# Optimization experiments

Measured on AMD Instinct MI355X. Metric: run time of the kernel, lower is better.

The kernel has to match this reference:

```python
import jax, jax.numpy as jnp
import numpy as np

ALPHA = 0.1
EPS = 1e-10

def setup_inputs() -> dict:
    key = jax.random.key(0)
    k1, k2 = jax.random.split(key)
    x = jax.random.normal(k1, (64, 8192, 128), dtype=jnp.float32)   # [B, N, D]
    pv = jax.random.uniform(k2, (64, 128), dtype=jnp.float32)        # [M, D] prototypes (torch.rand init)
    return {"x": x, "pv": pv}

def _cdist(x, pv):
    # Euclidean pairwise distance via GEMM form: [B,N,D] x [M,D] -> [B,N,M]
    x2 = jnp.sum(x * x, axis=-1, keepdims=True)          # [B,N,1]
    p2 = jnp.sum(pv * pv, axis=-1)                        # [M]
    xp = jnp.einsum('bnd,md->bnm', x, pv)                 # [B,N,M]
    return jnp.sqrt(jnp.maximum(x2 + p2 - 2.0 * xp, 0.0))

def reference(x, pv):
    dist = _cdist(x, pv)                                  # [B,N,M]
    min_dist = jnp.min(dist, axis=1)                      # [B,M] closest patch per prototype
    min_pos = jnp.argmin(dist, axis=1)                    # [B,M]
    # pick, per batch, the patch position of the globally closest prototype (no-grad in original)
    idx = jnp.argmin(min_dist, axis=1)                    # [B]
    min_pos = min_pos[jnp.arange(min_pos.shape[0]), idx]  # [B]
    max_sim = jnp.exp(EPS - ALPHA * min_dist)             # [B,M]
    return (max_sim, min_pos)
```

## Files before the change

### kernel.cpp

```cpp
#include <hip/hip_runtime.h>
#include <cfloat>
#include <cmath>

#define B_ 64
#define N_ 8192
#define D_ 128
#define M_ 64
#define CROWS 64
#define NCHUNK 4
#define BROWS (CROWS*NCHUNK)
#define NBLK (N_/BROWS)
#define ALPHA_ 0.1f
#define EPS_ 1e-10f

typedef __attribute__((ext_vector_type(4))) float f32x4;
typedef __attribute__((ext_vector_type(8))) short bf16x8;
typedef __attribute__((ext_vector_type(4))) short s16x4;

static __device__ __forceinline__ short f2bf(float f) {
    unsigned u = __float_as_uint(f);
    u += 0x7fff + ((u >> 16) & 1);
    return (short)(u >> 16);
}
static __device__ __forceinline__ float bf2f(short s) {
    return __uint_as_float(((unsigned)(unsigned short)s) << 16);
}

__global__ __launch_bounds__(256, 2)
void protomin_mfma(const float* __restrict__ x, const float* __restrict__ pv,
                   float* __restrict__ wsv, int* __restrict__ wsa) {
    __shared__ short xhi[2][CROWS * D_];
    __shared__ short xlo[2][CROWS * D_];
    __shared__ float x2s[2][CROWS];
    __shared__ float redv[2][M_];
    __shared__ int   redp[2][M_];

    const int tid = threadIdx.x;
    const int w   = tid >> 6;
    const int l   = tid & 63;
    const int lm  = l & 15, lg = l >> 4;
    const int wr  = w & 1;
    const int wm  = w >> 1;
    const int bid = blockIdx.x;
    const int b   = bid >> 5;
    const int nbase = (bid & 31) * BROWS;

    const float* xblk = x + ((size_t)b * N_ + nbase) * D_;

    f32x4 nv[8];
    {
        const f32x4* src = (const f32x4*)xblk;
#pragma unroll
        for (int i = 0; i < 8; ++i) nv[i] = src[(w * 8 + i) * 64 + l];
    }

    bf16x8 Bh[2][4], Bl[2][4];
#pragma unroll
    for (int mti = 0; mti < 2; ++mti) {
#pragma unroll
        for (int kt = 0; kt < 4; ++kt) {
            const float* p = pv + (wm * 32 + mti * 16 + lm) * D_ + kt * 32 + lg * 8;
            f32x4 p0 = *(const f32x4*)p;
            f32x4 p1 = *(const f32x4*)(p + 4);
#pragma unroll
            for (int j = 0; j < 4; ++j) {
                short h = f2bf(p0[j]);
                Bh[mti][kt][j] = h;
                Bl[mti][kt][j] = f2bf(p0[j] - bf2f(h));
            }
#pragma unroll
            for (int j = 0; j < 4; ++j) {
                short h = f2bf(p1[j]);
                Bh[mti][kt][4 + j] = h;
                Bl[mti][kt][4 + j] = f2bf(p1[j] - bf2f(h));
            }
        }
    }

    auto stage = [&](int buf) {
#pragma unroll
        for (int i = 0; i < 8; ++i) {
            int seg = w * 8 + i;
            int row = seg * 2 + (l >> 5);
            int ks  = (l & 31) * 4;
            f32x4 v = nv[i];
            float s = v[0] * v[0];
            s = fmaf(v[1], v[1], s); s = fmaf(v[2], v[2], s); s = fmaf(v[3], v[3], s);
            s += __shfl_xor(s, 1);  s += __shfl_xor(s, 2);  s += __shfl_xor(s, 4);
            s += __shfl_xor(s, 8);  s += __shfl_xor(s, 16);
            if ((l & 31) == 0) x2s[buf][row] = s;
            s16x4 hv, lv;
#pragma unroll
            for (int j = 0; j < 4; ++j) {
                short h = f2bf(v[j]);
                hv[j] = h;
                lv[j] = f2bf(v[j] - bf2f(h));
            }
            int sidx = row * D_ + (ks ^ ((row & 7) << 3));
            *(s16x4*)&xhi[buf][sidx] = hv;
            *(s16x4*)&xlo[buf][sidx] = lv;
        }
    };

    float bv[2]; int bp[2];
#pragma unroll
    for (int mti = 0; mti < 2; ++mti) { bv[mti] = FLT_MAX; bp[mti] = 0; }

    stage(0);
    __syncthreads();

    for (int c = 0; c < NCHUNK; ++c) {
        const int cur = c & 1;
        if (c + 1 < NCHUNK) {
            const f32x4* src = (const f32x4*)(xblk + (size_t)(c + 1) * CROWS * D_);
#pragma unroll
            for (int i = 0; i < 8; ++i) nv[i] = src[(w * 8 + i) * 64 + l];
        }

        f32x4 acc[2][2] = {};
#pragma unroll
        for (int kt = 0; kt < 4; ++kt) {
            bf16x8 ah[2], al[2];
#pragma unroll
            for (int rt = 0; rt < 2; ++rt) {
                int arow = wr * 32 + rt * 16 + lm;
                int koff = (kt * 32 + lg * 8) ^ ((arow & 7) << 3);
                ah[rt] = *(const bf16x8*)&xhi[cur][arow * D_ + koff];
                al[rt] = *(const bf16x8*)&xlo[cur][arow * D_ + koff];
            }
#pragma unroll
            for (int rt = 0; rt < 2; ++rt) {
#pragma unroll
                for (int mti = 0; mti < 2; ++mti) {
                    acc[rt][mti] = __builtin_amdgcn_mfma_f32_16x16x32_bf16(ah[rt], Bh[mti][kt], acc[rt][mti], 0, 0, 0);
                    acc[rt][mti] = __builtin_amdgcn_mfma_f32_16x16x32_bf16(al[rt], Bh[mti][kt], acc[rt][mti], 0, 0, 0);
                    acc[rt][mti] = __builtin_amdgcn_mfma_f32_16x16x32_bf16(ah[rt], Bl[mti][kt], acc[rt][mti], 0, 0, 0);
                    acc[rt][mti] = __builtin_amdgcn_mfma_f32_16x16x32_bf16(al[rt], Bl[mti][kt], acc[rt][mti], 0, 0, 0);
                }
            }
        }

#pragma unroll
        for (int rt = 0; rt < 2; ++rt) {
            const int rbase = wr * 32 + rt * 16 + lg * 4;
            float x2v[4];
#pragma unroll
            for (int r = 0; r < 4; ++r) x2v[r] = x2s[cur][rbase + r];
            const int npos0 = nbase + c * CROWS + rbase;
#pragma unroll
            for (int mti = 0; mti < 2; ++mti) {
#pragma unroll
                for (int r = 0; r < 4; ++r) {
                    float cand = fmaf(-2.f, acc[rt][mti][r], x2v[r]);
                    if (cand < bv[mti]) { bv[mti] = cand; bp[mti] = npos0 + r; }
                }
            }
        }

        if (c + 1 < NCHUNK) stage(cur ^ 1);
        __syncthreads();
    }

#pragma unroll
    for (int mti = 0; mti < 2; ++mti) {
        float v = bv[mti]; int p = bp[mti];
#pragma unroll
        for (int off = 16; off <= 32; off <<= 1) {
            float ov = __shfl_xor(v, off);
            int   op = __shfl_xor(p, off);
            if (ov < v || (ov == v && op < p)) { v = ov; p = op; }
        }
        if (l < 16) { redv[wr][wm * 32 + mti * 16 + l] = v;
                      redp[wr][wm * 32 + mti * 16 + l] = p; }
    }
    __syncthreads();

    if (tid < M_) {
        float v = redv[0][tid]; int p = redp[0][tid];
        float ov = redv[1][tid]; int op = redp[1][tid];
        if (ov < v || (ov == v && op < p)) { v = ov; p = op; }
        wsv[(size_t)bid * M_ + tid] = v;
        wsa[(size_t)bid * M_ + tid] = p;
    }
}

__global__ void finalize_kernel(const float* __restrict__ wsv,
                                const int* __restrict__ wsa,
                                const float* __restrict__ pv,
                                float* __restrict__ out) {
    const int b = blockIdx.x;
    const int m = threadIdx.x;

    float p2 = 0.f;
    const f32x4* pp = (const f32x4*)(pv + m * D_);
#pragma unroll 8
    for (int j = 0; j < 32; ++j) {
        f32x4 v = pp[j];
        p2 = fmaf(v[0], v[0], p2); p2 = fmaf(v[1], v[1], p2);
        p2 = fmaf(v[2], v[2], p2); p2 = fmaf(v[3], v[3], p2);
    }

    float v = FLT_MAX; int p = 0;
    for (int bc = 0; bc < NBLK; ++bc) {
        size_t idx = ((size_t)(b * NBLK + bc)) * M_ + m;
        float nv2 = wsv[idx]; int np = wsa[idx];
        if (nv2 < v || (nv2 == v && np < p)) { v = nv2; p = np; }
    }
    float dist = sqrtf(fmaxf(v + p2, 0.f));
    out[b * M_ + m] = expf(EPS_ - ALPHA_ * dist);

    __shared__ float sv[M_];
    __shared__ int   sa[M_];
    sv[m] = dist; sa[m] = p;
    __syncthreads();
    if (m == 0) {
        float best = FLT_MAX; int bpos = 0;
        for (int k = 0; k < M_; ++k)
            if (sv[k] < best) { best = sv[k]; bpos = sa[k]; }
        out[B_ * M_ + b] = (float)bpos;
    }
}

extern "C" void kernel_launch(void* const* d_in, const int* in_sizes, int n_in,
                              void* d_out, int out_size, void* d_ws, size_t ws_size,
                              hipStream_t stream) {
    const float* x  = (const float*)d_in[0];
    const float* pv = (const float*)d_in[1];
    float* out = (float*)d_out;

    float* wsv = (float*)d_ws;
    int*   wsa = (int*)((char*)d_ws + (size_t)B_ * NBLK * M_ * sizeof(float));

    hipLaunchKernelGGL(protomin_mfma, dim3(B_ * NBLK), dim3(256), 0, stream,
                       x, pv, wsv, wsa);
    hipLaunchKernelGGL(finalize_kernel, dim3(B_), dim3(M_), 0, stream,
                       wsv, wsa, pv, out);
}
```

Before: 377.3 us.

## Single-buffer LDS, drop lo*lo MFMA, truncating bf16 split, raise occupancy

Replaces the double-buffered LDS staging with a single buffer guarded by two barriers per chunk, which halves shared memory so three blocks per CU fit (launch bounds raised to 3). Drops the lo*lo MFMA term of the three-way bf16 split, cutting matrix work by a quarter. Replaces round-to-nearest bf16 conversion with bit truncation. The extra barrier serialises staging with compute, and the truncation plus the dropped term lower accuracy, which could flip argmin ties.

```diff
diff --git a/kernel.cpp b/kernel.cpp
--- a/kernel.cpp
+++ b/kernel.cpp
@@ -17,21 +17,12 @@
 typedef __attribute__((ext_vector_type(8))) short bf16x8;
 typedef __attribute__((ext_vector_type(4))) short s16x4;
 
-static __device__ __forceinline__ short f2bf(float f) {
-    unsigned u = __float_as_uint(f);
-    u += 0x7fff + ((u >> 16) & 1);
-    return (short)(u >> 16);
-}
-static __device__ __forceinline__ float bf2f(short s) {
-    return __uint_as_float(((unsigned)(unsigned short)s) << 16);
-}
-
-__global__ __launch_bounds__(256, 2)
+__global__ __launch_bounds__(256, 3)
 void protomin_mfma(const float* __restrict__ x, const float* __restrict__ pv,
                    float* __restrict__ wsv, int* __restrict__ wsa) {
-    __shared__ short xhi[2][CROWS * D_];
-    __shared__ short xlo[2][CROWS * D_];
-    __shared__ float x2s[2][CROWS];
+    __shared__ short xhi[CROWS * D_];
+    __shared__ short xlo[CROWS * D_];
+    __shared__ float x2s[CROWS];
     __shared__ float redv[2][M_];
     __shared__ int   redp[2][M_];
 
@@ -60,24 +51,22 @@
 #pragma unroll
         for (int kt = 0; kt < 4; ++kt) {
             const float* p = pv + (wm * 32 + mti * 16 + lm) * D_ + kt * 32 + lg * 8;
-            f32x4 p0 = *(const f32x4*)p;
-            f32x4 p1 = *(const f32x4*)(p + 4);
-#pragma unroll
-            for (int j = 0; j < 4; ++j) {
-                short h = f2bf(p0[j]);
-                Bh[mti][kt][j] = h;
-                Bl[mti][kt][j] = f2bf(p0[j] - bf2f(h));
-            }
-#pragma unroll
-            for (int j = 0; j < 4; ++j) {
-                short h = f2bf(p1[j]);
-                Bh[mti][kt][4 + j] = h;
-                Bl[mti][kt][4 + j] = f2bf(p1[j] - bf2f(h));
-            }
-        }
-    }
-
-    auto stage = [&](int buf) {
+#pragma unroll
+            for (int h = 0; h < 2; ++h) {
+                f32x4 pq = *(const f32x4*)(p + 4 * h);
+#pragma unroll
+                for (int j = 0; j < 4; ++j) {
+                    unsigned u = __float_as_uint(pq[j]);
+                    float hf = __uint_as_float(u & 0xffff0000u);
+                    Bh[mti][kt][4 * h + j] = (short)(u >> 16);
+                    float rem = pq[j] - hf;
+                    Bl[mti][kt][4 * h + j] = (short)(__float_as_uint(rem) >> 16);
+                }
+            }
+        }
+    }
+
+    auto stage = [&]() {
 #pragma unroll
         for (int i = 0; i < 8; ++i) {
             int seg = w * 8 + i;
@@ -88,17 +77,19 @@
             s = fmaf(v[1], v[1], s); s = fmaf(v[2], v[2], s); s = fmaf(v[3], v[3], s);
             s += __shfl_xor(s, 1);  s += __shfl_xor(s, 2);  s += __shfl_xor(s, 4);
             s += __shfl_xor(s, 8);  s += __shfl_xor(s, 16);
-            if ((l & 31) == 0) x2s[buf][row] = s;
+            if ((l & 31) == 0) x2s[row] = s;
             s16x4 hv, lv;
 #pragma unroll
             for (int j = 0; j < 4; ++j) {
-                short h = f2bf(v[j]);
-                hv[j] = h;
-                lv[j] = f2bf(v[j] - bf2f(h));
+                unsigned u = __float_as_uint(v[j]);
+                float hf = __uint_as_float(u & 0xffff0000u);
+                hv[j] = (short)(u >> 16);
+                float rem = v[j] - hf;
+                lv[j] = (short)(__float_as_uint(rem) >> 16);
             }
             int sidx = row * D_ + (ks ^ ((row & 7) << 3));
-            *(s16x4*)&xhi[buf][sidx] = hv;
-            *(s16x4*)&xlo[buf][sidx] = lv;
+            *(s16x4*)&xhi[sidx] = hv;
+            *(s16x4*)&xlo[sidx] = lv;
         }
     };
 
@@ -106,11 +97,10 @@
 #pragma unroll
     for (int mti = 0; mti < 2; ++mti) { bv[mti] = FLT_MAX; bp[mti] = 0; }
 
-    stage(0);
+    stage();
     __syncthreads();
 
     for (int c = 0; c < NCHUNK; ++c) {
-        const int cur = c & 1;
         if (c + 1 < NCHUNK) {
             const f32x4* src = (const f32x4*)(xblk + (size_t)(c + 1) * CROWS * D_);
 #pragma unroll
@@ -125,8 +115,8 @@
             for (int rt = 0; rt < 2; ++rt) {
                 int arow = wr * 32 + rt * 16 + lm;
                 int koff = (kt * 32 + lg * 8) ^ ((arow & 7) << 3);
-                ah[rt] = *(const bf16x8*)&xhi[cur][arow * D_ + koff];
-                al[rt] = *(const bf16x8*)&xlo[cur][arow * D_ + koff];
+                ah[rt] = *(const bf16x8*)&xhi[arow * D_ + koff];
+                al[rt] = *(const bf16x8*)&xlo[arow * D_ + koff];
             }
 #pragma unroll
             for (int rt = 0; rt < 2; ++rt) {
@@ -135,7 +125,6 @@
                     acc[rt][mti] = __builtin_amdgcn_mfma_f32_16x16x32_bf16(ah[rt], Bh[mti][kt], acc[rt][mti], 0, 0, 0);
                     acc[rt][mti] = __builtin_amdgcn_mfma_f32_16x16x32_bf16(al[rt], Bh[mti][kt], acc[rt][mti], 0, 0, 0);
                     acc[rt][mti] = __builtin_amdgcn_mfma_f32_16x16x32_bf16(ah[rt], Bl[mti][kt], acc[rt][mti], 0, 0, 0);
-                    acc[rt][mti] = __builtin_amdgcn_mfma_f32_16x16x32_bf16(al[rt], Bl[mti][kt], acc[rt][mti], 0, 0, 0);
                 }
             }
         }
@@ -145,7 +134,7 @@
             const int rbase = wr * 32 + rt * 16 + lg * 4;
             float x2v[4];
 #pragma unroll
-            for (int r = 0; r < 4; ++r) x2v[r] = x2s[cur][rbase + r];
+            for (int r = 0; r < 4; ++r) x2v[r] = x2s[rbase + r];
             const int npos0 = nbase + c * CROWS + rbase;
 #pragma unroll
             for (int mti = 0; mti < 2; ++mti) {
@@ -157,8 +146,11 @@
             }
         }
 
-        if (c + 1 < NCHUNK) stage(cur ^ 1);
-        __syncthreads();
+        if (c + 1 < NCHUNK) {
+            __syncthreads();
+            stage();
+            __syncthreads();
+        }
     }
 
 #pragma unroll
```

After: 378.5 us. Within noise of the previous version (+0.3%).
